# Performance work log

Measured on AMD Instinct MI355X. Metric: run time of the kernel, lower is better.

The kernel has to match this reference:

```python
import jax, jax.numpy as jnp
import numpy as np

N = 50000      # nodes
E = 800000     # edges
F_IN = 128     # input_dim
H = 4          # GAT heads
C = 32         # hidden_dim (per head)
HC = H * C     # 128, concat GAT output
NG = 64        # graphs in batch
OUT = 10       # classes


def _gat_conv(x, src, dst, W, att_src, att_dst, bias):
    # PyG GATConv (concat=True, add_self_loops=True, negative_slope=0.2)
    n = x.shape[0]
    h = (x @ W).reshape(n, H, -1)                      # [N,H,C]
    a_s = (h * att_src).sum(-1)                        # [N,H]
    a_d = (h * att_dst).sum(-1)                        # [N,H]
    loop = jnp.arange(n)
    s = jnp.concatenate([src, loop])                   # self-loops appended
    d = jnp.concatenate([dst, loop])
    e = jax.nn.leaky_relu(a_s[s] + a_d[d], 0.2)        # [E+N,H]
    m = jax.ops.segment_max(e, d, num_segments=n)
    e = jnp.exp(e - m[d])
    z = jax.ops.segment_sum(e, d, num_segments=n)
    alpha = e / (z[d] + 1e-16)                         # edge softmax per dst,head
    out = jax.ops.segment_sum(h[s] * alpha[..., None], d, num_segments=n)
    return out.reshape(n, -1) + bias                   # [N,H*C]


def setup_inputs() -> dict:
    key = jax.random.key(0)
    ks = jax.random.split(key, 20)
    g = lambda k, shp, fan: jax.random.normal(k, shp, jnp.float32) / np.sqrt(fan)
    inp = {
        'x': jax.random.normal(ks[0], (N, F_IN), jnp.float32),
        'edge_index': jax.random.randint(ks[1], (2, E), 0, N),
        'batch': jnp.sort(jax.random.randint(ks[2], (N,), 0, NG)),
        # GATConv 1: F_IN -> H*C
        'W1': g(ks[3], (F_IN, HC), F_IN),
        'as1': g(ks[4], (H, C), C), 'ad1': g(ks[5], (H, C), C),
        'b1': jnp.zeros((HC,), jnp.float32),
        # GATConv 2: H*C -> H*C
        'W2': g(ks[6], (HC, HC), HC),
        'as2': g(ks[7], (H, C), C), 'ad2': g(ks[8], (H, C), C),
        'b2': jnp.zeros((HC,), jnp.float32),
        # GraphConv: H*C -> C  (lin_rel has bias, lin_root does not)
        'W3r': g(ks[9], (HC, C), HC), 'W3l': g(ks[10], (HC, C), HC),
        'b3': jnp.zeros((C,), jnp.float32),
        # SAGEConv: C -> C (mean aggr; lin_l has bias, lin_r does not)
        'W4l': g(ks[11], (C, C), C), 'b4l': jnp.zeros((C,), jnp.float32),
        'W4r': g(ks[12], (C, C), C),
        # MLP head
        'Wf1': g(ks[13], (C, C), C), 'bf1': jnp.zeros((C,), jnp.float32),
        'Wf2': g(ks[14], (C, OUT), C), 'bf2': jnp.zeros((OUT,), jnp.float32),
    }
    return inp


def reference(x, edge_index, batch, W1, as1, ad1, b1, W2, as2, ad2, b2,
              W3r, W3l, b3, W4l, b4l, W4r, Wf1, bf1, Wf2, bf2):
    src, dst = edge_index[0], edge_index[1]
    relu = jax.nn.relu
    n = x.shape[0]
    # GAT layers (dropout is identity in eval)
    x = relu(_gat_conv(x, src, dst, W1, as1, ad1, b1))
    x = relu(_gat_conv(x, src, dst, W2, as2, ad2, b2))
    # GraphConv: lin_rel(sum_neighbors) + lin_root(x)
    agg = jax.ops.segment_sum(x[src], dst, num_segments=n)
    x = relu(agg @ W3r + b3 + x @ W3l)
    # SAGEConv: lin_l(mean_neighbors) + lin_r(x)
    deg = jax.ops.segment_sum(jnp.ones((src.shape[0],), x.dtype), dst, num_segments=n)
    mean = jax.ops.segment_sum(x[src], dst, num_segments=n) / jnp.maximum(deg, 1.0)[:, None]
    x = relu(mean @ W4l + b4l + x @ W4r)
    # global mean pool over graphs
    cnt = jax.ops.segment_sum(jnp.ones((n,), x.dtype), batch, num_segments=NG)
    gpool = jax.ops.segment_sum(x, batch, num_segments=NG) / jnp.maximum(cnt, 1.0)[:, None]
    gpool = relu(gpool @ Wf1 + bf1)
    return gpool @ Wf2 + bf2
```

## Files before the change

### kernel.cpp

```cpp
#include <hip/hip_runtime.h>
#include <hip/hip_bf16.h>
#include <type_traits>


typedef __bf16 v8bf __attribute__((ext_vector_type(8)));
typedef float  v4f  __attribute__((ext_vector_type(4)));

__device__ __forceinline__ float lrelu(float x) { return x > 0.f ? x : 0.2f * x; }

__device__ __forceinline__ unsigned short f2bf(float f) {
    unsigned u = __float_as_uint(f);
    unsigned r = (u + 0x7FFF + ((u >> 16) & 1)) >> 16;
    return (unsigned short)r;
}
__device__ __forceinline__ float bfbits2f(unsigned short u) {
    return __uint_as_float((unsigned)u << 16);
}
__device__ __forceinline__ float bflo(int v) { return __uint_as_float((unsigned)v << 16); }
__device__ __forceinline__ float bfhi(int v) { return __uint_as_float((unsigned)v & 0xffff0000u); }
__device__ __forceinline__ int packbf2(float a, float b) {
    return (int)f2bf(a) | ((int)f2bf(b) << 16);
}

__device__ __forceinline__ void fma8(float* acc, int4 u, float w) {
    acc[0] += w * bflo(u.x); acc[1] += w * bfhi(u.x);
    acc[2] += w * bflo(u.y); acc[3] += w * bfhi(u.y);
    acc[4] += w * bflo(u.z); acc[5] += w * bfhi(u.z);
    acc[6] += w * bflo(u.w); acc[7] += w * bfhi(u.w);
}


__global__ __launch_bounds__(256) void bucket_hist(const int* __restrict__ dst,
                                                   int* __restrict__ bcount,
                                                   int E, int nbuck) {
    __shared__ int hist[256];
    int t = threadIdx.x;
    for (int i = t; i < nbuck; i += 256) hist[i] = 0;
    __syncthreads();
    int base = blockIdx.x * 4096;
    #pragma unroll
    for (int k = 0; k < 16; ++k) {
        int e = base + k * 256 + t;
        if (e < E) atomicAdd(&hist[dst[e] >> 8], 1);
    }
    __syncthreads();
    for (int i = t; i < nbuck; i += 256) {
        int c = hist[i];
        if (c) atomicAdd(&bcount[i], c);
    }
}

__global__ __launch_bounds__(256) void scan_convert(
    const int* __restrict__ bcount, int* __restrict__ bbase, int* __restrict__ gcursor,
    int nbuck, int E, int* __restrict__ rowptr, int n,
    const float* __restrict__ W1, const float* __restrict__ W2,
    const float* __restrict__ W3r, const float* __restrict__ W3l,
    const float* __restrict__ as1, const float* __restrict__ ad1,
    const float* __restrict__ as2, const float* __restrict__ ad2,
    __hip_bfloat16* __restrict__ W1t, __hip_bfloat16* __restrict__ W2t,
    __hip_bfloat16* __restrict__ W3rt, __hip_bfloat16* __restrict__ W3lt)
{
    int t = threadIdx.x;
    if (blockIdx.x == 0) {
        __shared__ int red[256];
        int v = (t < nbuck) ? bcount[t] : 0;
        red[t] = v;
        __syncthreads();
        for (int off = 1; off < 256; off <<= 1) {
            int u = (t >= off) ? red[t - off] : 0;
            __syncthreads();
            red[t] += u;
            __syncthreads();
        }
        int ex = red[t] - v;
        if (t < nbuck) { bbase[t] = ex; gcursor[t] = ex; }
        if (t == 0) { bbase[nbuck] = E; rowptr[n] = E; }
        return;
    }
    int b = blockIdx.x - 1;
    int i = b * 256 + t;
    {
        int k = i >> 7, c = i & 127;
        *(unsigned short*)&W1t[c * 128 + k] = f2bf(W1[i]);
        *(unsigned short*)&W2t[c * 128 + k] = f2bf(W2[i]);
    }
    if (i < 4096) {
        int k = i >> 5, c = i & 31;
        *(unsigned short*)&W3rt[c * 128 + k] = f2bf(W3r[i]);
        *(unsigned short*)&W3lt[c * 128 + k] = f2bf(W3l[i]);
    }
    if (b == 0) {
        for (int u = t; u < 512; u += 256) {
            int k = u & 127, hd = u >> 7;
            float vs1 = 0.f, vd1 = 0.f, vs2 = 0.f, vd2 = 0.f;
            #pragma unroll
            for (int j = 0; j < 32; ++j) {
                int c = hd * 32 + j;
                float w1 = W1[k * 128 + c], w2 = W2[k * 128 + c];
                vs1 += w1 * as1[c]; vd1 += w1 * ad1[c];
                vs2 += w2 * as2[c]; vd2 += w2 * ad2[c];
            }
            unsigned short h1s = f2bf(vs1), h1d = f2bf(vd1);
            unsigned short h2s = f2bf(vs2), h2d = f2bf(vd2);
            *(unsigned short*)&W1t[(128 + hd) * 128 + k] = h1s;
            *(unsigned short*)&W1t[(132 + hd) * 128 + k] = f2bf(vs1 - bfbits2f(h1s));
            *(unsigned short*)&W1t[(136 + hd) * 128 + k] = h1d;
            *(unsigned short*)&W1t[(140 + hd) * 128 + k] = f2bf(vd1 - bfbits2f(h1d));
            *(unsigned short*)&W2t[(128 + hd) * 128 + k] = h2s;
            *(unsigned short*)&W2t[(132 + hd) * 128 + k] = f2bf(vs2 - bfbits2f(h2s));
            *(unsigned short*)&W2t[(136 + hd) * 128 + k] = h2d;
            *(unsigned short*)&W2t[(140 + hd) * 128 + k] = f2bf(vd2 - bfbits2f(h2d));
        }
    }
}

__global__ __launch_bounds__(256) void bucket_scatter(const int* __restrict__ dst,
                                                      const int* __restrict__ src,
                                                      int* __restrict__ gcursor,
                                                      int* __restrict__ pairs,
                                                      int E, int nbuck) {
    __shared__ int hist[256], lcur[256];
    int t = threadIdx.x;
    for (int i = t; i < nbuck; i += 256) hist[i] = 0;
    __syncthreads();
    int base = blockIdx.x * 2048;
    int dreg[8];
    #pragma unroll
    for (int k = 0; k < 8; ++k) {
        int e = base + k * 256 + t;
        int d = (e < E) ? dst[e] : -1;
        dreg[k] = d;
        if (d >= 0) atomicAdd(&hist[d >> 8], 1);
    }
    __syncthreads();
    for (int i = t; i < nbuck; i += 256) {
        int c = hist[i];
        lcur[i] = c ? atomicAdd(&gcursor[i], c) : 0;
    }
    __syncthreads();
    #pragma unroll
    for (int k = 0; k < 8; ++k) {
        int e = base + k * 256 + t;
        if (e < E) {
            int d = dreg[k];
            int p = atomicAdd(&lcur[d >> 8], 1);
            pairs[p] = ((d & 255) << 17) | src[e];
        }
    }
}

__global__ __launch_bounds__(256) void bucket_fill(const int* __restrict__ pairs,
                                                   const int* __restrict__ bbase,
                                                   int* __restrict__ rowptr,
                                                   int* __restrict__ colsrc, int n) {
    __shared__ int deg[256], excl[256], cur[256];
    int b = blockIdx.x, t = threadIdx.x;
    int e0 = bbase[b], e1 = bbase[b + 1];
    int d0 = b << 8;
    deg[t] = 0;
    __syncthreads();
    for (int j = e0 + t; j < e1; j += 256)
        atomicAdd(&deg[pairs[j] >> 17], 1);
    __syncthreads();
    int v = deg[t];
    excl[t] = v;
    __syncthreads();
    for (int off = 1; off < 256; off <<= 1) {
        int u = (t >= off) ? excl[t - off] : 0;
        __syncthreads();
        excl[t] += u;
        __syncthreads();
    }
    int base = e0 + excl[t] - v;
    if (d0 + t < n) rowptr[d0 + t] = base;
    cur[t] = base;
    __syncthreads();
    for (int j = e0 + t; j < e1; j += 256) {
        int w = pairs[j];
        int p = atomicAdd(&cur[w >> 17], 1);
        colsrc[p] = w & 0x1FFFF;
    }
}

template <typename T>
__global__ __launch_bounds__(256) void gemm_att_mfma(
    const T* __restrict__ X, const __hip_bfloat16* __restrict__ Wt,
    __hip_bfloat16* __restrict__ h, float* __restrict__ a_s, float* __restrict__ a_d, int n)
{
    __shared__ __align__(16) __hip_bfloat16 sWt[144 * 136];
    int t = threadIdx.x;
    for (int i = t; i < 144 * 16; i += 256) {
        int row = i >> 4, chh = i & 15;
        *(int4*)&sWt[row * 136 + chh * 8] = *(const int4*)&Wt[row * 128 + chh * 8];
    }
    __syncthreads();
    int wave = t >> 6, lane = t & 63, quad = lane >> 4, l16 = lane & 15;

    v8bf z;
    #pragma unroll
    for (int i = 0; i < 8; ++i) z[i] = (__bf16)0.f;

    int nrb = (n + 15) >> 4;
    for (int rb = blockIdx.x * 4 + wave; rb < nrb; rb += gridDim.x * 4) {
        int rowbase = rb * 16;
        int arow = rowbase + l16;
        bool ok = arow < n;
        v8bf af[4];
        if constexpr (std::is_same<T, float>::value) {
            const float* xf = X + (size_t)(ok ? arow : 0) * 128;
            #pragma unroll
            for (int ks = 0; ks < 4; ++ks) {
                if (ok) {
                    float4 u = *(const float4*)&xf[ks * 32 + quad * 8];
                    float4 v = *(const float4*)&xf[ks * 32 + quad * 8 + 4];
                    v8bf a;
                    unsigned short r;
                    r = f2bf(u.x); a[0] = *(__bf16*)&r;
                    r = f2bf(u.y); a[1] = *(__bf16*)&r;
                    r = f2bf(u.z); a[2] = *(__bf16*)&r;
                    r = f2bf(u.w); a[3] = *(__bf16*)&r;
                    r = f2bf(v.x); a[4] = *(__bf16*)&r;
                    r = f2bf(v.y); a[5] = *(__bf16*)&r;
                    r = f2bf(v.z); a[6] = *(__bf16*)&r;
                    r = f2bf(v.w); a[7] = *(__bf16*)&r;
                    af[ks] = a;
                } else af[ks] = z;
            }
        } else {
            const v8bf* px = (const v8bf*)(X + (size_t)(ok ? arow : 0) * 128);
            #pragma unroll
            for (int ks = 0; ks < 4; ++ks) af[ks] = ok ? px[ks * 4 + quad] : z;
        }

        v4f acc[9];
        #pragma unroll
        for (int ct = 0; ct < 9; ++ct) acc[ct] = (v4f){0.f, 0.f, 0.f, 0.f};
        #pragma unroll
        for (int ct = 0; ct < 9; ++ct) {
            #pragma unroll
            for (int ks = 0; ks < 4; ++ks) {
                v8bf b = *(const v8bf*)&sWt[(ct * 16 + l16) * 136 + ks * 32 + quad * 8];
                acc[ct] = __builtin_amdgcn_mfma_f32_16x16x32_bf16(af[ks], b, acc[ct], 0, 0, 0);
            }
        }

        #pragma unroll
        for (int reg = 0; reg < 4; ++reg) {
            int r = rowbase + quad * 4 + reg;
            if (r < n) {
                #pragma unroll
                for (int ct = 0; ct < 8; ++ct)
                    *(unsigned short*)&h[(size_t)r * 128 + ct * 16 + l16] = f2bf(acc[ct][reg]);
            }
        }
        #pragma unroll
        for (int reg = 0; reg < 4; ++reg) {
            float v = acc[8][reg] + __shfl_xor(acc[8][reg], 4);
            int r = rowbase + quad * 4 + reg;
            if (r < n) {
                if (l16 < 4)                    a_s[r * 4 + l16] = v;
                else if (l16 >= 8 && l16 < 12)  a_d[r * 4 + (l16 - 8)] = v;
            }
        }
    }
}

__global__ __launch_bounds__(256) void gat_aggr(
    const __hip_bfloat16* __restrict__ h, const float* __restrict__ a_s,
    const float* __restrict__ a_d,
    const int* __restrict__ rowptr, const int* __restrict__ colsrc,
    const float* __restrict__ bias, __hip_bfloat16* __restrict__ out, int n)
{
    __shared__ float s_w[4][64 * 4];
    int t = threadIdx.x;
    int wave = t >> 6, lane = t & 63;
    int d = blockIdx.x * 4 + wave;
    if (d >= n) d = n - 1;
    int beg = rowptr[d], end = rowptr[d + 1];
    int cnt = end - beg;
    float4 ad4 = *(const float4*)&a_d[d * 4];
    float4 asd = *(const float4*)&a_s[d * 4];
    float es0 = lrelu(asd.x + ad4.x), es1 = lrelu(asd.y + ad4.y);
    float es2 = lrelu(asd.z + ad4.z), es3 = lrelu(asd.w + ad4.w);

    int l16 = lane & 15, egrp = lane >> 4;
    int ch = l16 * 8;
    int head = l16 >> 2;
    const char* hb = (const char*)h;
    unsigned chb = (unsigned)(ch << 1);

    float acc[8];
    #pragma unroll
    for (int i = 0; i < 8; ++i) acc[i] = 0.f;
    float zp = 0.f;

    for (int j0 = 0; j0 < cnt; j0 += 64) {
        int ne = min(64, cnt - j0);
        float w0 = 0.f, w1 = 0.f, w2 = 0.f, w3 = 0.f;
        int s = 0;
        if (lane < ne) {
            s = colsrc[beg + j0 + lane];
            float4 sv = *(const float4*)&a_s[s * 4];
            w0 = __expf(lrelu(sv.x + ad4.x));
            w1 = __expf(lrelu(sv.y + ad4.y));
            w2 = __expf(lrelu(sv.z + ad4.z));
            w3 = __expf(lrelu(sv.w + ad4.w));
        }
        float4 wv = {w0, w1, w2, w3};
        *(float4*)&s_w[wave][lane * 4] = wv;
        __asm volatile("s_waitcnt lgkmcnt(0)" ::: "memory");
        int kmax = (ne + 3) >> 2;
        int k = 0;
        for (; k + 4 <= kmax; k += 4) {
            int jb = egrp + 4 * k;
            int ss0 = __shfl(s, jb);
            int ss1 = __shfl(s, jb + 4);
            int ss2 = __shfl(s, jb + 8);
            int ss3 = __shfl(s, jb + 12);
            float wj0 = s_w[wave][jb * 4 + head];
            float wj1 = s_w[wave][(jb + 4) * 4 + head];
            float wj2 = s_w[wave][(jb + 8) * 4 + head];
            float wj3 = s_w[wave][(jb + 12) * 4 + head];
            int4 u0 = *(const int4*)(hb + (((unsigned)ss0 << 8) + chb));
            int4 u1 = *(const int4*)(hb + (((unsigned)ss1 << 8) + chb));
            int4 u2 = *(const int4*)(hb + (((unsigned)ss2 << 8) + chb));
            int4 u3 = *(const int4*)(hb + (((unsigned)ss3 << 8) + chb));
            zp += (wj0 + wj1) + (wj2 + wj3);
            fma8(acc, u0, wj0);
            fma8(acc, u1, wj1);
            fma8(acc, u2, wj2);
            fma8(acc, u3, wj3);
        }
        for (; k + 2 <= kmax; k += 2) {
            int jb = egrp + 4 * k;
            int ss0 = __shfl(s, jb);
            int ss1 = __shfl(s, jb + 4);
            float wj0 = s_w[wave][jb * 4 + head];
            float wj1 = s_w[wave][(jb + 4) * 4 + head];
            int4 u0 = *(const int4*)(hb + (((unsigned)ss0 << 8) + chb));
            int4 u1 = *(const int4*)(hb + (((unsigned)ss1 << 8) + chb));
            zp += wj0 + wj1;
            fma8(acc, u0, wj0);
            fma8(acc, u1, wj1);
        }
        if (k < kmax) {
            int jb = egrp + 4 * k;
            int ss0 = __shfl(s, jb);
            float wj0 = s_w[wave][jb * 4 + head];
            int4 u0 = *(const int4*)(hb + (((unsigned)ss0 << 8) + chb));
            zp += wj0;
            fma8(acc, u0, wj0);
        }
    }

    int4 hu = {0, 0, 0, 0};
    float4 b0 = {0.f, 0.f, 0.f, 0.f}, b1 = {0.f, 0.f, 0.f, 0.f};
    if (egrp == 0) {
        hu = *(const int4*)(hb + (((unsigned)d << 8) + chb));
        b0 = *(const float4*)&bias[ch];
        b1 = *(const float4*)&bias[ch + 4];
    }
    #pragma unroll
    for (int off = 16; off < 64; off <<= 1) {
        zp += __shfl_xor(zp, off);
        #pragma unroll
        for (int i = 0; i < 8; ++i) acc[i] += __shfl_xor(acc[i], off);
    }

    if (egrp == 0) {
        float eh = (head < 2) ? (head == 0 ? es0 : es1) : (head == 2 ? es2 : es3);
        float ws = __expf(eh);
        float inv = 1.f / (zp + ws + 1e-16f);
        float hs[8] = {bflo(hu.x), bfhi(hu.x), bflo(hu.y), bfhi(hu.y),
                       bflo(hu.z), bfhi(hu.z), bflo(hu.w), bfhi(hu.w)};
        float o[8];
        o[0] = fmaxf((acc[0] + ws * hs[0]) * inv + b0.x, 0.f);
        o[1] = fmaxf((acc[1] + ws * hs[1]) * inv + b0.y, 0.f);
        o[2] = fmaxf((acc[2] + ws * hs[2]) * inv + b0.z, 0.f);
        o[3] = fmaxf((acc[3] + ws * hs[3]) * inv + b0.w, 0.f);
        o[4] = fmaxf((acc[4] + ws * hs[4]) * inv + b1.x, 0.f);
        o[5] = fmaxf((acc[5] + ws * hs[5]) * inv + b1.y, 0.f);
        o[6] = fmaxf((acc[6] + ws * hs[6]) * inv + b1.z, 0.f);
        o[7] = fmaxf((acc[7] + ws * hs[7]) * inv + b1.w, 0.f);
        int4 ou;
        ou.x = packbf2(o[0], o[1]); ou.y = packbf2(o[2], o[3]);
        ou.z = packbf2(o[4], o[5]); ou.w = packbf2(o[6], o[7]);
        *(int4*)&out[(size_t)d * 128 + ch] = ou;
    }
}

__global__ __launch_bounds__(256) void graphconv_lin(
    const __hip_bfloat16* __restrict__ Xb,
    const __hip_bfloat16* __restrict__ Wrt, const __hip_bfloat16* __restrict__ Wlt,
    const float* __restrict__ bias, __hip_bfloat16* __restrict__ y,
    float* __restrict__ root, int n)
{
    __shared__ __align__(16) __hip_bfloat16 sWr[32 * 136], sWl[32 * 136];
    int t = threadIdx.x;
    for (int i = t; i < 32 * 16; i += 256) {
        int row = i >> 4, chh = i & 15;
        *(int4*)&sWr[row * 136 + chh * 8] = *(const int4*)&Wrt[row * 128 + chh * 8];
        *(int4*)&sWl[row * 136 + chh * 8] = *(const int4*)&Wlt[row * 128 + chh * 8];
    }
    __syncthreads();
    int wave = t >> 6, lane = t & 63, quad = lane >> 4, l16 = lane & 15;

    v8bf z;
    #pragma unroll
    for (int i = 0; i < 8; ++i) z[i] = (__bf16)0.f;

    int nrb = (n + 15) >> 4;
    for (int rb = blockIdx.x * 4 + wave; rb < nrb; rb += gridDim.x * 4) {
        int rowbase = rb * 16;
        int arow = rowbase + l16;
        bool ok = arow < n;
        const v8bf* px = (const v8bf*)(Xb + (size_t)(ok ? arow : 0) * 128);
        v8bf fx[4];
        #pragma unroll
        for (int ks = 0; ks < 4; ++ks) fx[ks] = ok ? px[ks * 4 + quad] : z;

        v4f accR[2], accL[2];
        #pragma unroll
        for (int ct = 0; ct < 2; ++ct) {
            accR[ct] = (v4f){0.f, 0.f, 0.f, 0.f};
            accL[ct] = (v4f){0.f, 0.f, 0.f, 0.f};
            #pragma unroll
            for (int ks = 0; ks < 4; ++ks) {
                v8bf br = *(const v8bf*)&sWr[(ct * 16 + l16) * 136 + ks * 32 + quad * 8];
                accR[ct] = __builtin_amdgcn_mfma_f32_16x16x32_bf16(fx[ks], br, accR[ct], 0, 0, 0);
                v8bf bl = *(const v8bf*)&sWl[(ct * 16 + l16) * 136 + ks * 32 + quad * 8];
                accL[ct] = __builtin_amdgcn_mfma_f32_16x16x32_bf16(fx[ks], bl, accL[ct], 0, 0, 0);
            }
        }
        #pragma unroll
        for (int ct = 0; ct < 2; ++ct) {
            float bcol = bias[ct * 16 + l16];
            #pragma unroll
            for (int reg = 0; reg < 4; ++reg) {
                int r = rowbase + quad * 4 + reg;
                if (r < n) {
                    *(unsigned short*)&y[(size_t)r * 32 + ct * 16 + l16] = f2bf(accR[ct][reg]);
                    root[(size_t)r * 32 + ct * 16 + l16] = accL[ct][reg] + bcol;
                }
            }
        }
    }
}

__global__ __launch_bounds__(256) void graphconv_aggr(
    const __hip_bfloat16* __restrict__ y, const float* __restrict__ root,
    const int* __restrict__ rowptr, const int* __restrict__ colsrc,
    __hip_bfloat16* __restrict__ x3, int n)
{
    int t = threadIdx.x;
    int wave = t >> 6, lane = t & 63;
    int d = blockIdx.x * 4 + wave;
    if (d >= n) d = n - 1;
    int beg = rowptr[d], end = rowptr[d + 1];
    int cnt = end - beg;
    int l4 = lane & 3, egrp = lane >> 2;
    int ch = l4 * 8;
    float acc[8];
    #pragma unroll
    for (int i = 0; i < 8; ++i) acc[i] = 0.f;
    for (int j0 = 0; j0 < cnt; j0 += 64) {
        int ne = min(64, cnt - j0);
        int s = (lane < ne) ? colsrc[beg + j0 + lane] : 0;
        int kmax = (ne + 15) >> 4;
        #pragma unroll 2
        for (int k = 0; k < kmax; ++k) {
            int j = egrp + 16 * k;
            int ss = __shfl(s, j);
            float m = (j < ne) ? 1.f : 0.f;
            int4 u = *(const int4*)&y[(size_t)ss * 32 + ch];
            acc[0] += m * bflo(u.x); acc[1] += m * bfhi(u.x);
            acc[2] += m * bflo(u.y); acc[3] += m * bfhi(u.y);
            acc[4] += m * bflo(u.z); acc[5] += m * bfhi(u.z);
            acc[6] += m * bflo(u.w); acc[7] += m * bfhi(u.w);
        }
    }
    float4 r0 = {0.f, 0.f, 0.f, 0.f}, r1 = {0.f, 0.f, 0.f, 0.f};
    if (egrp == 0) {
        r0 = *(const float4*)&root[(size_t)d * 32 + ch];
        r1 = *(const float4*)&root[(size_t)d * 32 + ch + 4];
    }
    #pragma unroll
    for (int off = 4; off < 64; off <<= 1)
        #pragma unroll
        for (int i = 0; i < 8; ++i) acc[i] += __shfl_xor(acc[i], off);
    if (egrp == 0) {
        float o[8];
        o[0] = fmaxf(acc[0] + r0.x, 0.f); o[1] = fmaxf(acc[1] + r0.y, 0.f);
        o[2] = fmaxf(acc[2] + r0.z, 0.f); o[3] = fmaxf(acc[3] + r0.w, 0.f);
        o[4] = fmaxf(acc[4] + r1.x, 0.f); o[5] = fmaxf(acc[5] + r1.y, 0.f);
        o[6] = fmaxf(acc[6] + r1.z, 0.f); o[7] = fmaxf(acc[7] + r1.w, 0.f);
        int4 ou;
        ou.x = packbf2(o[0], o[1]); ou.y = packbf2(o[2], o[3]);
        ou.z = packbf2(o[4], o[5]); ou.w = packbf2(o[6], o[7]);
        *(int4*)&x3[(size_t)d * 32 + ch] = ou;
    }
}

__global__ __launch_bounds__(256) void mean_aggr32(
    const __hip_bfloat16* __restrict__ x, const int* __restrict__ rowptr,
    const int* __restrict__ colsrc, float* __restrict__ mean, int n)
{
    int t = threadIdx.x;
    int wave = t >> 6, lane = t & 63;
    int d = blockIdx.x * 4 + wave;
    if (d >= n) d = n - 1;
    int beg = rowptr[d], end = rowptr[d + 1];
    int cnt = end - beg;
    int l4 = lane & 3, egrp = lane >> 2;
    int ch = l4 * 8;
    float acc[8];
    #pragma unroll
    for (int i = 0; i < 8; ++i) acc[i] = 0.f;
    for (int j0 = 0; j0 < cnt; j0 += 64) {
        int ne = min(64, cnt - j0);
        int s = (lane < ne) ? colsrc[beg + j0 + lane] : 0;
        int kmax = (ne + 15) >> 4;
        #pragma unroll 2
        for (int k = 0; k < kmax; ++k) {
            int j = egrp + 16 * k;
            int ss = __shfl(s, j);
            float m = (j < ne) ? 1.f : 0.f;
            int4 u = *(const int4*)&x[(size_t)ss * 32 + ch];
            acc[0] += m * bflo(u.x); acc[1] += m * bfhi(u.x);
            acc[2] += m * bflo(u.y); acc[3] += m * bfhi(u.y);
            acc[4] += m * bflo(u.z); acc[5] += m * bfhi(u.z);
            acc[6] += m * bflo(u.w); acc[7] += m * bfhi(u.w);
        }
    }
    #pragma unroll
    for (int off = 4; off < 64; off <<= 1)
        #pragma unroll
        for (int i = 0; i < 8; ++i) acc[i] += __shfl_xor(acc[i], off);
    if (egrp == 0) {
        float invd = 1.f / fmaxf((float)cnt, 1.f);
        float4 lo = {acc[0] * invd, acc[1] * invd, acc[2] * invd, acc[3] * invd};
        float4 hi = {acc[4] * invd, acc[5] * invd, acc[6] * invd, acc[7] * invd};
        *(float4*)&mean[(size_t)d * 32 + ch]     = lo;
        *(float4*)&mean[(size_t)d * 32 + ch + 4] = hi;
    }
}

__global__ __launch_bounds__(256) void sage_gemm(
    const float* __restrict__ mean, const __hip_bfloat16* __restrict__ xin,
    const float* __restrict__ Wl, const float* __restrict__ bl,
    const float* __restrict__ Wr, float* __restrict__ out, int n)
{
    __shared__ __align__(16) float sWl[32 * 32], sWr[32 * 32];
    __shared__ __align__(16) float sm[8 * 32], sx[8 * 32];
    int t = threadIdx.x;
    for (int i = t; i < 1024; i += 256) { sWl[i] = Wl[i]; sWr[i] = Wr[i]; }
    int c = t & 31, rr = t >> 5;
    float bc = bl[c];
    for (int row0 = blockIdx.x * 8; row0 < n; row0 += gridDim.x * 8) {
        __syncthreads();
        {
            int i = t;
            int r = i >> 5, cc = i & 31;
            int row = row0 + r;
            sm[i] = (row < n) ? mean[row * 32 + cc] : 0.f;
            sx[i] = (row < n) ? bfbits2f(*(const unsigned short*)&xin[row * 32 + cc]) : 0.f;
        }
        __syncthreads();
        float acc = bc;
        const float4* pm = (const float4*)&sm[rr * 32];
        const float4* px = (const float4*)&sx[rr * 32];
        #pragma unroll
        for (int k4 = 0; k4 < 8; ++k4) {
            float4 vm = pm[k4], vx = px[k4];
            const float* wl = &sWl[(k4 * 4) * 32 + c];
            const float* wr = &sWr[(k4 * 4) * 32 + c];
            acc += vm.x * wl[0] + vm.y * wl[32] + vm.z * wl[64] + vm.w * wl[96];
            acc += vx.x * wr[0] + vx.y * wr[32] + vx.z * wr[64] + vx.w * wr[96];
        }
        int row = row0 + rr;
        if (row < n) out[row * 32 + c] = fmaxf(acc, 0.f);
    }
}

__device__ __forceinline__ int lower_bound_i(const int* a, int n, int key) {
    int lo = 0, hi = n;
    while (lo < hi) { int mid = (lo + hi) >> 1; if (a[mid] < key) lo = mid + 1; else hi = mid; }
    return lo;
}

__global__ __launch_bounds__(256) void pool_kernel(
    const float* __restrict__ x, const int* __restrict__ batch,
    float* __restrict__ gpool, int n)
{
    int g = blockIdx.x;
    int lo = lower_bound_i(batch, n, g);
    int hi = lower_bound_i(batch, n, g + 1);
    int t = threadIdx.x;
    int c = t & 31, rr = t >> 5;
    float acc = 0.f;
    for (int i = lo + rr; i < hi; i += 8) acc += x[i * 32 + c];
    __shared__ float sred[256];
    sred[t] = acc;
    __syncthreads();
    if (t < 128) sred[t] += sred[t + 128];
    __syncthreads();
    if (t < 64) sred[t] += sred[t + 64];
    __syncthreads();
    if (t < 32) {
        float v = sred[t] + sred[t + 32];
        gpool[g * 32 + t] = v / fmaxf((float)(hi - lo), 1.f);
    }
}

__global__ __launch_bounds__(256) void head_kernel(
    const float* __restrict__ gpool, const float* __restrict__ Wf1, const float* __restrict__ bf1,
    const float* __restrict__ Wf2, const float* __restrict__ bf2, float* __restrict__ out)
{
    __shared__ float sg[64 * 32], st[64 * 32];
    __shared__ float sW1[32 * 32], sW2[32 * 10];
    int t = threadIdx.x;
    for (int i = t; i < 2048; i += 256) sg[i] = gpool[i];
    for (int i = t; i < 1024; i += 256) sW1[i] = Wf1[i];
    for (int i = t; i < 320; i += 256) sW2[i] = Wf2[i];
    __syncthreads();
    for (int i = t; i < 2048; i += 256) {
        int g = i >> 5, c = i & 31;
        float acc = bf1[c];
        #pragma unroll
        for (int k = 0; k < 32; ++k) acc += sg[g * 32 + k] * sW1[k * 32 + c];
        st[i] = fmaxf(acc, 0.f);
    }
    __syncthreads();
    for (int i = t; i < 640; i += 256) {
        int g = i / 10, o = i - g * 10;
        float acc = bf2[o];
        #pragma unroll
        for (int k = 0; k < 32; ++k) acc += st[g * 32 + k] * sW2[k * 10 + o];
        out[i] = acc;
    }
}

extern "C" void kernel_launch(void* const* d_in, const int* in_sizes, int n_in,
                              void* d_out, int out_size, void* d_ws, size_t ws_size,
                              hipStream_t stream) {
    const float* x    = (const float*)d_in[0];
    const int*   ei   = (const int*)d_in[1];
    const int*   batch= (const int*)d_in[2];
    const float* W1   = (const float*)d_in[3];
    const float* as1  = (const float*)d_in[4];
    const float* ad1  = (const float*)d_in[5];
    const float* b1   = (const float*)d_in[6];
    const float* W2   = (const float*)d_in[7];
    const float* as2  = (const float*)d_in[8];
    const float* ad2  = (const float*)d_in[9];
    const float* b2   = (const float*)d_in[10];
    const float* W3r  = (const float*)d_in[11];
    const float* W3l  = (const float*)d_in[12];
    const float* b3   = (const float*)d_in[13];
    const float* W4l  = (const float*)d_in[14];
    const float* b4l  = (const float*)d_in[15];
    const float* W4r  = (const float*)d_in[16];
    const float* Wf1  = (const float*)d_in[17];
    const float* bf1  = (const float*)d_in[18];
    const float* Wf2  = (const float*)d_in[19];
    const float* bf2  = (const float*)d_in[20];

    const int N = in_sizes[0] / 128;
    const int E = in_sizes[1] / 2;
    const int* src = ei;
    const int* dst = ei + E;

    char* p = (char*)d_ws;
    auto alloc = [&](size_t bytes) -> void* {
        void* r = (void*)p;
        p += (bytes + 255) & ~(size_t)255;
        return r;
    };
    __hip_bfloat16* buf1 = (__hip_bfloat16*)alloc((size_t)N * 128 * 2);
    __hip_bfloat16* buf2 = (__hip_bfloat16*)alloc((size_t)N * 128 * 2);
    __hip_bfloat16* buf3 = (__hip_bfloat16*)alloc((size_t)N * 128 * 2);
    float* aS     = (float*)alloc((size_t)N * 4 * 4);
    float* aD     = (float*)alloc((size_t)N * 4 * 4);
    int*   rowptr = (int*)alloc((size_t)(N + 1) * 4);
    int*   colsrc = (int*)alloc((size_t)E * 4);
    int*   bcount = (int*)alloc(256 * 4);
    int*   bbase  = (int*)alloc(257 * 4);
    int*   gcursor= (int*)alloc(256 * 4);
    __hip_bfloat16* W1t  = (__hip_bfloat16*)alloc(144 * 128 * 2);
    __hip_bfloat16* W2t  = (__hip_bfloat16*)alloc(144 * 128 * 2);
    __hip_bfloat16* W3rt = (__hip_bfloat16*)alloc(32 * 128 * 2);
    __hip_bfloat16* W3lt = (__hip_bfloat16*)alloc(32 * 128 * 2);
    float* gpool  = (float*)alloc(64 * 32 * 4);

    __hip_bfloat16* X3b  = buf2;
    float*          MEAN = (float*)((char*)buf2 + (((size_t)N * 32 * 2 + 255) & ~(size_t)255));
    float*          X4   = (float*)buf1;
    __hip_bfloat16* Y32  = buf3;
    float*          ROOT = (float*)((char*)buf3 + (((size_t)N * 32 * 2 + 255) & ~(size_t)255));
    int*            pairs = (int*)buf3;

    const int nbuck = (N + 255) >> 8;

    hipMemsetAsync(bcount, 0, 256 * 4, stream);
    bucket_hist<<<(E + 4095) / 4096, 256, 0, stream>>>(dst, bcount, E, nbuck);
    scan_convert<<<65, 256, 0, stream>>>(bcount, bbase, gcursor, nbuck, E, rowptr, N,
                                         W1, W2, W3r, W3l, as1, ad1, as2, ad2,
                                         W1t, W2t, W3rt, W3lt);
    bucket_scatter<<<(E + 2047) / 2048, 256, 0, stream>>>(dst, src, gcursor, pairs, E, nbuck);
    bucket_fill<<<nbuck, 256, 0, stream>>>(pairs, bbase, rowptr, colsrc, N);

    int gmm = (N + 63) / 64;
    if (gmm > 320) gmm = 320;
    const int gag = (N + 3) / 4;
    gemm_att_mfma<float><<<gmm, 256, 0, stream>>>(x, W1t, buf3, aS, aD, N);
    gat_aggr<<<gag, 256, 0, stream>>>(buf3, aS, aD, rowptr, colsrc, b1, buf2, N);
    gemm_att_mfma<__hip_bfloat16><<<gmm, 256, 0, stream>>>(buf2, W2t, buf3, aS, aD, N);
    gat_aggr<<<gag, 256, 0, stream>>>(buf3, aS, aD, rowptr, colsrc, b2, buf1, N);
    graphconv_lin<<<gmm, 256, 0, stream>>>(buf1, W3rt, W3lt, b3, Y32, ROOT, N);
    graphconv_aggr<<<gag, 256, 0, stream>>>(Y32, ROOT, rowptr, colsrc, X3b, N);
    mean_aggr32<<<gag, 256, 0, stream>>>(X3b, rowptr, colsrc, MEAN, N);
    sage_gemm<<<1024, 256, 0, stream>>>(MEAN, X3b, W4l, b4l, W4r, X4, N);
    pool_kernel<<<64, 256, 0, stream>>>(X4, batch, gpool, N);
    head_kernel<<<1, 256, 0, stream>>>(gpool, Wf1, bf1, Wf2, bf2, (float*)d_out);
}
```

Baseline: 356.2 us.

## Pack multiple destination nodes per wavefront in GAT and neighbor aggregation kernels

The GAT aggregation kernel now gives each half-wave its own destination node, so one wave handles two nodes instead of one. The GraphConv and mean aggregation kernels now give each 16-lane quarter-wave its own node. With an average degree of about 16, one node per 64-lane wave left most lanes idle, and packing nodes raises lane utilization and cuts the number of blocks and cross-lane reductions. The cost is that lanes sharing a wave run to the maximum degree among the packed nodes, which causes divergence and wasted iterations when degrees differ.

After: 328.9 us. 7.7% less time.

```diff
diff --git a/kernel.cpp b/kernel.cpp
--- a/kernel.cpp
+++ b/kernel.cpp
@@ -271,35 +271,39 @@
     const int* __restrict__ rowptr, const int* __restrict__ colsrc,
     const float* __restrict__ bias, __hip_bfloat16* __restrict__ out, int n)
 {
-    __shared__ float s_w[4][64 * 4];
+    __shared__ float s_w[4][2 * 32 * 4];
     int t = threadIdx.x;
     int wave = t >> 6, lane = t & 63;
-    int d = blockIdx.x * 4 + wave;
+    int half = lane >> 5, hl = lane & 31;
+    int d = blockIdx.x * 8 + wave * 2 + half;
     if (d >= n) d = n - 1;
     int beg = rowptr[d], end = rowptr[d + 1];
     int cnt = end - beg;
+    int cmax = max(cnt, __shfl_xor(cnt, 32));
     float4 ad4 = *(const float4*)&a_d[d * 4];
     float4 asd = *(const float4*)&a_s[d * 4];
     float es0 = lrelu(asd.x + ad4.x), es1 = lrelu(asd.y + ad4.y);
     float es2 = lrelu(asd.z + ad4.z), es3 = lrelu(asd.w + ad4.w);
 
-    int l16 = lane & 15, egrp = lane >> 4;
+    int egrp = hl >> 4, l16 = hl & 15;
     int ch = l16 * 8;
     int head = l16 >> 2;
     const char* hb = (const char*)h;
     unsigned chb = (unsigned)(ch << 1);
+    int sbase = half * 128;
+    int lbase = half * 32;
 
     float acc[8];
     #pragma unroll
     for (int i = 0; i < 8; ++i) acc[i] = 0.f;
     float zp = 0.f;
 
-    for (int j0 = 0; j0 < cnt; j0 += 64) {
-        int ne = min(64, cnt - j0);
+    for (int j0 = 0; j0 < cmax; j0 += 32) {
+        int ne = cnt - j0;
         float w0 = 0.f, w1 = 0.f, w2 = 0.f, w3 = 0.f;
         int s = 0;
-        if (lane < ne) {
-            s = colsrc[beg + j0 + lane];
+        if (hl < ne) {
+            s = colsrc[beg + j0 + hl];
             float4 sv = *(const float4*)&a_s[s * 4];
             w0 = __expf(lrelu(sv.x + ad4.x));
             w1 = __expf(lrelu(sv.y + ad4.y));
@@ -307,20 +311,21 @@
             w3 = __expf(lrelu(sv.w + ad4.w));
         }
         float4 wv = {w0, w1, w2, w3};
-        *(float4*)&s_w[wave][lane * 4] = wv;
+        *(float4*)&s_w[wave][sbase + hl * 4] = wv;
         __asm volatile("s_waitcnt lgkmcnt(0)" ::: "memory");
-        int kmax = (ne + 3) >> 2;
+        int nemax = cmax - j0; if (nemax > 32) nemax = 32;
+        int kmax = (nemax + 1) >> 1;
         int k = 0;
         for (; k + 4 <= kmax; k += 4) {
-            int jb = egrp + 4 * k;
-            int ss0 = __shfl(s, jb);
-            int ss1 = __shfl(s, jb + 4);
-            int ss2 = __shfl(s, jb + 8);
-            int ss3 = __shfl(s, jb + 12);
-            float wj0 = s_w[wave][jb * 4 + head];
-            float wj1 = s_w[wave][(jb + 4) * 4 + head];
-            float wj2 = s_w[wave][(jb + 8) * 4 + head];
-            float wj3 = s_w[wave][(jb + 12) * 4 + head];
+            int jb = egrp + 2 * k;
+            int ss0 = __shfl(s, lbase + jb);
+            int ss1 = __shfl(s, lbase + jb + 2);
+            int ss2 = __shfl(s, lbase + jb + 4);
+            int ss3 = __shfl(s, lbase + jb + 6);
+            float wj0 = s_w[wave][sbase + jb * 4 + head];
+            float wj1 = s_w[wave][sbase + (jb + 2) * 4 + head];
+            float wj2 = s_w[wave][sbase + (jb + 4) * 4 + head];
+            float wj3 = s_w[wave][sbase + (jb + 6) * 4 + head];
             int4 u0 = *(const int4*)(hb + (((unsigned)ss0 << 8) + chb));
             int4 u1 = *(const int4*)(hb + (((unsigned)ss1 << 8) + chb));
             int4 u2 = *(const int4*)(hb + (((unsigned)ss2 << 8) + chb));
@@ -332,11 +337,11 @@
             fma8(acc, u3, wj3);
         }
         for (; k + 2 <= kmax; k += 2) {
-            int jb = egrp + 4 * k;
-            int ss0 = __shfl(s, jb);
-            int ss1 = __shfl(s, jb + 4);
-            float wj0 = s_w[wave][jb * 4 + head];
-            float wj1 = s_w[wave][(jb + 4) * 4 + head];
+            int jb = egrp + 2 * k;
+            int ss0 = __shfl(s, lbase + jb);
+            int ss1 = __shfl(s, lbase + jb + 2);
+            float wj0 = s_w[wave][sbase + jb * 4 + head];
+            float wj1 = s_w[wave][sbase + (jb + 2) * 4 + head];
             int4 u0 = *(const int4*)(hb + (((unsigned)ss0 << 8) + chb));
             int4 u1 = *(const int4*)(hb + (((unsigned)ss1 << 8) + chb));
             zp += wj0 + wj1;
@@ -344,9 +349,9 @@
             fma8(acc, u1, wj1);
         }
         if (k < kmax) {
-            int jb = egrp + 4 * k;
-            int ss0 = __shfl(s, jb);
-            float wj0 = s_w[wave][jb * 4 + head];
+            int jb = egrp + 2 * k;
+            int ss0 = __shfl(s, lbase + jb);
+            float wj0 = s_w[wave][sbase + jb * 4 + head];
             int4 u0 = *(const int4*)(hb + (((unsigned)ss0 << 8) + chb));
             zp += wj0;
             fma8(acc, u0, wj0);
@@ -360,12 +365,9 @@
         b0 = *(const float4*)&bias[ch];
         b1 = *(const float4*)&bias[ch + 4];
     }
-    #pragma unroll
-    for (int off = 16; off < 64; off <<= 1) {
-        zp += __shfl_xor(zp, off);
-        #pragma unroll
-        for (int i = 0; i < 8; ++i) acc[i] += __shfl_xor(acc[i], off);
-    }
+    zp += __shfl_xor(zp, 16);
+    #pragma unroll
+    for (int i = 0; i < 8; ++i) acc[i] += __shfl_xor(acc[i], 16);
 
     if (egrp == 0) {
         float eh = (head < 2) ? (head == 0 ? es0 : es1) : (head == 2 ? es2 : es3);
@@ -454,29 +456,42 @@
 {
     int t = threadIdx.x;
     int wave = t >> 6, lane = t & 63;
-    int d = blockIdx.x * 4 + wave;
+    int qr = lane >> 4, hl = lane & 15;
+    int d = blockIdx.x * 16 + wave * 4 + qr;
     if (d >= n) d = n - 1;
-    int beg = rowptr[d], end = rowptr[d + 1];
-    int cnt = end - beg;
-    int l4 = lane & 3, egrp = lane >> 2;
+    int beg = rowptr[d];
+    int cnt = rowptr[d + 1] - beg;
+    int cm = max(cnt, __shfl_xor(cnt, 16));
+    cm = max(cm, __shfl_xor(cm, 32));
+    int l4 = hl & 3, egrp = hl >> 2;
     int ch = l4 * 8;
+    int lbase = qr * 16;
     float acc[8];
     #pragma unroll
     for (int i = 0; i < 8; ++i) acc[i] = 0.f;
-    for (int j0 = 0; j0 < cnt; j0 += 64) {
-        int ne = min(64, cnt - j0);
-        int s = (lane < ne) ? colsrc[beg + j0 + lane] : 0;
-        int kmax = (ne + 15) >> 4;
-        #pragma unroll 2
-        for (int k = 0; k < kmax; ++k) {
-            int j = egrp + 16 * k;
-            int ss = __shfl(s, j);
-            float m = (j < ne) ? 1.f : 0.f;
-            int4 u = *(const int4*)&y[(size_t)ss * 32 + ch];
-            acc[0] += m * bflo(u.x); acc[1] += m * bfhi(u.x);
-            acc[2] += m * bflo(u.y); acc[3] += m * bfhi(u.y);
-            acc[4] += m * bflo(u.z); acc[5] += m * bfhi(u.z);
-            acc[6] += m * bflo(u.w); acc[7] += m * bfhi(u.w);
+    for (int j0 = 0; j0 < cm; j0 += 16) {
+        int ne = cnt - j0;
+        int s = (hl < ne) ? colsrc[beg + j0 + hl] : 0;
+        int nemax = cm - j0; if (nemax > 16) nemax = 16;
+        int kmax = (nemax + 3) >> 2;
+        int k = 0;
+        for (; k + 2 <= kmax; k += 2) {
+            int ja = egrp + 4 * k, jb = ja + 4;
+            int sa = __shfl(s, lbase + ja);
+            int sb = __shfl(s, lbase + jb);
+            float ma = (ja < ne) ? 1.f : 0.f;
+            float mb = (jb < ne) ? 1.f : 0.f;
+            int4 ua = *(const int4*)&y[(size_t)sa * 32 + ch];
+            int4 ub = *(const int4*)&y[(size_t)sb * 32 + ch];
+            fma8(acc, ua, ma);
+            fma8(acc, ub, mb);
+        }
+        if (k < kmax) {
+            int ja = egrp + 4 * k;
+            int sa = __shfl(s, lbase + ja);
+            float ma = (ja < ne) ? 1.f : 0.f;
+            int4 ua = *(const int4*)&y[(size_t)sa * 32 + ch];
+            fma8(acc, ua, ma);
         }
     }
     float4 r0 = {0.f, 0.f, 0.f, 0.f}, r1 = {0.f, 0.f, 0.f, 0.f};
@@ -485,7 +500,7 @@
         r1 = *(const float4*)&root[(size_t)d * 32 + ch + 4];
     }
     #pragma unroll
-    for (int off = 4; off < 64; off <<= 1)
+    for (int off = 4; off < 16; off <<= 1)
         #pragma unroll
         for (int i = 0; i < 8; ++i) acc[i] += __shfl_xor(acc[i], off);
     if (egrp == 0) {
@@ -507,33 +522,46 @@
 {
     int t = threadIdx.x;
     int wave = t >> 6, lane = t & 63;
-    int d = blockIdx.x * 4 + wave;
+    int qr = lane >> 4, hl = lane & 15;
+    int d = blockIdx.x * 16 + wave * 4 + qr;
     if (d >= n) d = n - 1;
-    int beg = rowptr[d], end = rowptr[d + 1];
-    int cnt = end - beg;
-    int l4 = lane & 3, egrp = lane >> 2;
+    int beg = rowptr[d];
+    int cnt = rowptr[d + 1] - beg;
+    int cm = max(cnt, __shfl_xor(cnt, 16));
+    cm = max(cm, __shfl_xor(cm, 32));
+    int l4 = hl & 3, egrp = hl >> 2;
     int ch = l4 * 8;
+    int lbase = qr * 16;
     float acc[8];
     #pragma unroll
     for (int i = 0; i < 8; ++i) acc[i] = 0.f;
-    for (int j0 = 0; j0 < cnt; j0 += 64) {
-        int ne = min(64, cnt - j0);
-        int s = (lane < ne) ? colsrc[beg + j0 + lane] : 0;
-        int kmax = (ne + 15) >> 4;
-        #pragma unroll 2
-        for (int k = 0; k < kmax; ++k) {
-            int j = egrp + 16 * k;
-            int ss = __shfl(s, j);
-            float m = (j < ne) ? 1.f : 0.f;
-            int4 u = *(const int4*)&x[(size_t)ss * 32 + ch];
-            acc[0] += m * bflo(u.x); acc[1] += m * bfhi(u.x);
-            acc[2] += m * bflo(u.y); acc[3] += m * bfhi(u.y);
-            acc[4] += m * bflo(u.z); acc[5] += m * bfhi(u.z);
-            acc[6] += m * bflo(u.w); acc[7] += m * bfhi(u.w);
-        }
-    }
-    #pragma unroll
-    for (int off = 4; off < 64; off <<= 1)
+    for (int j0 = 0; j0 < cm; j0 += 16) {
+        int ne = cnt - j0;
+        int s = (hl < ne) ? colsrc[beg + j0 + hl] : 0;
+        int nemax = cm - j0; if (nemax > 16) nemax = 16;
+        int kmax = (nemax + 3) >> 2;
+        int k = 0;
+        for (; k + 2 <= kmax; k += 2) {
+            int ja = egrp + 4 * k, jb = ja + 4;
+            int sa = __shfl(s, lbase + ja);
+            int sb = __shfl(s, lbase + jb);
+            float ma = (ja < ne) ? 1.f : 0.f;
+            float mb = (jb < ne) ? 1.f : 0.f;
+            int4 ua = *(const int4*)&x[(size_t)sa * 32 + ch];
+            int4 ub = *(const int4*)&x[(size_t)sb * 32 + ch];
+            fma8(acc, ua, ma);
+            fma8(acc, ub, mb);
+        }
+        if (k < kmax) {
+            int ja = egrp + 4 * k;
+            int sa = __shfl(s, lbase + ja);
+            float ma = (ja < ne) ? 1.f : 0.f;
+            int4 ua = *(const int4*)&x[(size_t)sa * 32 + ch];
+            fma8(acc, ua, ma);
+        }
+    }
+    #pragma unroll
+    for (int off = 4; off < 16; off <<= 1)
         #pragma unroll
         for (int i = 0; i < 8; ++i) acc[i] += __shfl_xor(acc[i], off);
     if (egrp == 0) {
@@ -711,14 +739,15 @@
 
     int gmm = (N + 63) / 64;
     if (gmm > 320) gmm = 320;
-    const int gag = (N + 3) / 4;
+    const int gag2 = (N + 7) / 8;
+    const int gag4 = (N + 15) / 16;
     gemm_att_mfma<float><<<gmm, 256, 0, stream>>>(x, W1t, buf3, aS, aD, N);
-    gat_aggr<<<gag, 256, 0, stream>>>(buf3, aS, aD, rowptr, colsrc, b1, buf2, N);
+    gat_aggr<<<gag2, 256, 0, stream>>>(buf3, aS, aD, rowptr, colsrc, b1, buf2, N);
     gemm_att_mfma<__hip_bfloat16><<<gmm, 256, 0, stream>>>(buf2, W2t, buf3, aS, aD, N);
-    gat_aggr<<<gag, 256, 0, stream>>>(buf3, aS, aD, rowptr, colsrc, b2, buf1, N);
+    gat_aggr<<<gag2, 256, 0, stream>>>(buf3, aS, aD, rowptr, colsrc, b2, buf1, N);
     graphconv_lin<<<gmm, 256, 0, stream>>>(buf1, W3rt, W3lt, b3, Y32, ROOT, N);
-    graphconv_aggr<<<gag, 256, 0, stream>>>(Y32, ROOT, rowptr, colsrc, X3b, N);
-    mean_aggr32<<<gag, 256, 0, stream>>>(X3b, rowptr, colsrc, MEAN, N);
+    graphconv_aggr<<<gag4, 256, 0, stream>>>(Y32, ROOT, rowptr, colsrc, X3b, N);
+    mean_aggr32<<<gag4, 256, 0, stream>>>(X3b, rowptr, colsrc, MEAN, N);
     sage_gemm<<<1024, 256, 0, stream>>>(MEAN, X3b, W4l, b4l, W4r, X4, N);
     pool_kernel<<<64, 256, 0, stream>>>(X4, batch, gpool, N);
     head_kernel<<<1, 256, 0, stream>>>(gpool, Wf1, bf1, Wf2, bf2, (float*)d_out);
```
